# Kernel tuning notes

Hardware: AMD Instinct MI355X
Metric: run time of the kernel (lower is better)

## Reference

```python
import jax, jax.numpy as jnp
import numpy as np

N_NODES = 100000
N_EDGES = 300000
D_IN = 256
HID = 1024
N_CLASSES = 64


def _linear_params(key, d_in, d_out):
    k1, k2 = jax.random.split(key)
    bound = 1.0 / np.sqrt(d_in)
    W = jax.random.uniform(k1, (d_in, d_out), jnp.float32, -bound, bound)
    b = jax.random.uniform(k2, (d_out,), jnp.float32, -bound, bound)
    return W, b


def setup_inputs() -> dict:
    key = jax.random.key(0)
    ks = jax.random.split(key, 8)
    x = jax.random.normal(ks[0], (N_NODES, D_IN), jnp.float32)
    edge_index = jax.random.randint(ks[1], (2, N_EDGES), 0, N_NODES, jnp.int64)
    W1a, b1a = _linear_params(ks[2], D_IN, HID)
    W1b, b1b = _linear_params(ks[3], HID, HID)
    W2a, b2a = _linear_params(ks[4], HID, HID)
    W2b, b2b = _linear_params(ks[5], HID, HID)
    Wfc, bfc = _linear_params(ks[6], HID, N_CLASSES)
    return {"x": x, "edge_index": edge_index,
            "W1a": W1a, "b1a": b1a, "W1b": W1b, "b1b": b1b,
            "W2a": W2a, "b2a": b2a, "W2b": W2b, "b2b": b2b,
            "Wfc": Wfc, "bfc": bfc}


def _gin_conv(x, src, dst, Wa, ba, Wb, bb):
    # GINConv, eps=0: nn(x + sum_{j in N(i)} x_j); messages flow src -> dst.
    agg = jax.ops.segment_sum(x[src], dst, num_segments=N_NODES)
    h = x + agg
    h = jax.nn.relu(h @ Wa + ba)
    return h @ Wb + bb


def reference(x, edge_index, W1a, b1a, W1b, b1b, W2a, b2a, W2b, b2b, Wfc, bfc):
    src, dst = edge_index[0], edge_index[1]
    h = _gin_conv(x, src, dst, W1a, b1a, W1b, b1b)
    h = jax.nn.relu(h)
    h = _gin_conv(h, src, dst, W2a, b2a, W2b, b2b)
    logits = h @ Wfc + bfc
    return jax.nn.log_softmax(logits, axis=1)
```

## Files before the change

kernel.cpp:

```cpp
#include <hip/hip_runtime.h>
#include <stdint.h>

#define N_NODES 100000
#define N_EDGES 300000
#define D_IN 256
#define HID 1024
#define N_CLASSES 64
#define NSCAN ((N_NODES + 1023) / 1024)

typedef __bf16 bf16x8 __attribute__((ext_vector_type(8)));
typedef float f32x4 __attribute__((ext_vector_type(4)));

__device__ __forceinline__ float bf2f(unsigned short u) {
  union { unsigned int i; float f; } v; v.i = ((unsigned int)u) << 16; return v.f;
}
__device__ __forceinline__ unsigned short f2bf(float f) {
  union { float f; unsigned int i; } v; v.f = f;
  unsigned int u = v.i;
  unsigned int r = (u + 0x7FFFu + ((u >> 16) & 1u)) >> 16;
  return (unsigned short)r;
}

__device__ __forceinline__ void async16(const void* g, void* l) {
  __builtin_amdgcn_global_load_lds(
      (const __attribute__((address_space(1))) void*)g,
      (__attribute__((address_space(3))) void*)l, 16, 0, 0);
}

__global__ void probe_flags(const unsigned short* __restrict__ w,
                            const unsigned int* __restrict__ e,
                            int* __restrict__ flags) {
  __shared__ int cnt;
  __shared__ unsigned int orv;
  if (threadIdx.x == 0) { cnt = 0; orv = 0u; }
  __syncthreads();
  int c = 0;
  for (int i = threadIdx.x; i < 4096; i += 256) {
    unsigned int ex = (w[i] >> 7) & 0xFFu;
    if (ex > 123u) ++c;
  }
  atomicAdd(&cnt, c);
  unsigned int o = 0;
  for (int j = threadIdx.x; j < 1000; j += 256) o |= e[2 * j + 1];
  atomicOr(&orv, o);
  __syncthreads();
  if (threadIdx.x == 0) {
    flags[0] = (cnt > 64) ? 1 : 0;
    flags[1] = (orv == 0u) ? 1 : 0;
  }
}

__global__ void cvt_edges(const unsigned int* __restrict__ ei,
                          int* __restrict__ src32, int* __restrict__ dst32,
                          const int* __restrict__ flags) {
  int i = blockIdx.x * 256 + threadIdx.x;
  if (i >= N_EDGES) return;
  if (flags[1]) {
    src32[i] = (int)ei[2 * i];
    dst32[i] = (int)ei[2 * (size_t)N_EDGES + 2 * i];
  } else {
    src32[i] = (int)ei[i];
    dst32[i] = (int)ei[N_EDGES + i];
  }
}

template <int FB16>
__global__ void transpose_tile(const void* __restrict__ W,
                               unsigned short* __restrict__ Wt, int K, int N,
                               const int* __restrict__ flags) {
  __shared__ float t[64][65];
  const int n0 = blockIdx.x * 64, k0 = blockIdx.y * 64;
  const int lane = threadIdx.x & 63, rg = threadIdx.x >> 6;
  const bool isf32 = FB16 ? false : (flags[0] != 0);
#pragma unroll
  for (int i = 0; i < 16; ++i) {
    int r = rg * 16 + i;
    long idx = (long)(k0 + r) * N + n0 + lane;
    t[r][lane] = isf32 ? ((const float*)W)[idx]
                       : bf2f(((const unsigned short*)W)[idx]);
  }
  __syncthreads();
#pragma unroll
  for (int i = 0; i < 16; ++i) {
    int r = rg * 16 + i;
    Wt[(long)(n0 + r) * K + k0 + lane] = f2bf(t[lane][r]);
  }
}

__global__ void cvt_bias_all(const void* __restrict__ b1a, const void* __restrict__ b1b,
                             const void* __restrict__ b2a, const void* __restrict__ b2b,
                             const void* __restrict__ bfc,
                             unsigned short* __restrict__ bb,
                             const int* __restrict__ flags) {
  int i = blockIdx.x * 256 + threadIdx.x;
  if (i >= 4 * HID + N_CLASSES) return;
  const void* src; int off;
  if (i < HID)          { src = b1a; off = i; }
  else if (i < 2 * HID) { src = b1b; off = i - HID; }
  else if (i < 3 * HID) { src = b2a; off = i - 2 * HID; }
  else if (i < 4 * HID) { src = b2b; off = i - 3 * HID; }
  else                  { src = bfc; off = i - 4 * HID; }
  bb[i] = flags[0] ? f2bf(((const float*)src)[off])
                   : ((const unsigned short*)src)[off];
}

__global__ void bcomb_kernel(const unsigned short* __restrict__ bb2b,
                             const unsigned short* __restrict__ WfcT,
                             const unsigned short* __restrict__ bbfc,
                             unsigned short* __restrict__ bcomb) {
  int c = threadIdx.x;
  if (c >= N_CLASSES) return;
  float s = bf2f(bbfc[c]);
  for (int j = 0; j < HID; ++j)
    s += bf2f(bb2b[j]) * bf2f(WfcT[(long)c * HID + j]);
  bcomb[c] = f2bf(s);
}

__global__ void hist_deg(const int* __restrict__ dst, int* __restrict__ deg) {
  int e = blockIdx.x * 256 + threadIdx.x;
  if (e < N_EDGES) atomicAdd(&deg[dst[e]], 1);
}

__global__ void scan_part(const int* __restrict__ deg, int* __restrict__ rowptr,
                          int* __restrict__ bsum) {
  __shared__ int lds[1024];
  int i = blockIdx.x * 1024 + threadIdx.x;
  int v = (i < N_NODES) ? deg[i] : 0;
  lds[threadIdx.x] = v;
  __syncthreads();
  for (int off = 1; off < 1024; off <<= 1) {
    int t = (threadIdx.x >= off) ? lds[threadIdx.x - off] : 0;
    __syncthreads();
    lds[threadIdx.x] += t;
    __syncthreads();
  }
  if (i < N_NODES) rowptr[i + 1] = lds[threadIdx.x];
  if (threadIdx.x == 1023) bsum[blockIdx.x] = lds[1023];
}

__global__ void scan_top(int* __restrict__ bsum) {
  __shared__ int lds[128];
  int v = (threadIdx.x < NSCAN) ? bsum[threadIdx.x] : 0;
  lds[threadIdx.x] = v;
  __syncthreads();
  for (int off = 1; off < 128; off <<= 1) {
    int t = (threadIdx.x >= off) ? lds[threadIdx.x - off] : 0;
    __syncthreads();
    lds[threadIdx.x] += t;
    __syncthreads();
  }
  if (threadIdx.x < NSCAN) bsum[threadIdx.x] = lds[threadIdx.x] - v;
}

__global__ void scan_fix(const int* __restrict__ deg, int* __restrict__ rowptr,
                         int* __restrict__ cursor, const int* __restrict__ bsum) {
  int i = blockIdx.x * 1024 + threadIdx.x;
  if (i < N_NODES) {
    int incl = rowptr[i + 1] + bsum[blockIdx.x];
    rowptr[i + 1] = incl;
    cursor[i] = incl - deg[i];
  }
  if (i == 0) rowptr[0] = 0;
}

__global__ void fill_csr(const int* __restrict__ src, const int* __restrict__ dst,
                         int* __restrict__ cursor, int* __restrict__ csr) {
  int e = blockIdx.x * 256 + threadIdx.x;
  if (e < N_EDGES) {
    int pos = atomicAdd(&cursor[dst[e]], 1);
    csr[pos] = src[e];
  }
}

__global__ void agg1_full(const void* __restrict__ X,
                          const int* __restrict__ rowptr,
                          const int* __restrict__ csr,
                          unsigned short* __restrict__ h,
                          const int* __restrict__ flags) {
  int node = blockIdx.x * 4 + (threadIdx.x >> 6);
  int lane = threadIdx.x & 63;
  if (node >= N_NODES) return;
  bool isf32 = flags[0] != 0;
  float acc[4];
  int e0 = rowptr[node], e1 = rowptr[node + 1];
  if (isf32) {
    const float* Xf = (const float*)X;
    float4 v = ((const float4*)(Xf + (long)node * D_IN))[lane];
    acc[0] = v.x; acc[1] = v.y; acc[2] = v.z; acc[3] = v.w;
    int j = e0;
    for (; j + 3 < e1; j += 4) {
      int s0 = csr[j], s1 = csr[j + 1], s2 = csr[j + 2], s3 = csr[j + 3];
      float4 v0 = ((const float4*)(Xf + (long)s0 * D_IN))[lane];
      float4 v1 = ((const float4*)(Xf + (long)s1 * D_IN))[lane];
      float4 v2 = ((const float4*)(Xf + (long)s2 * D_IN))[lane];
      float4 v3 = ((const float4*)(Xf + (long)s3 * D_IN))[lane];
      acc[0] += v0.x; acc[1] += v0.y; acc[2] += v0.z; acc[3] += v0.w;
      acc[0] += v1.x; acc[1] += v1.y; acc[2] += v1.z; acc[3] += v1.w;
      acc[0] += v2.x; acc[1] += v2.y; acc[2] += v2.z; acc[3] += v2.w;
      acc[0] += v3.x; acc[1] += v3.y; acc[2] += v3.z; acc[3] += v3.w;
    }
    for (; j < e1; ++j) {
      int s = csr[j];
      float4 v0 = ((const float4*)(Xf + (long)s * D_IN))[lane];
      acc[0] += v0.x; acc[1] += v0.y; acc[2] += v0.z; acc[3] += v0.w;
    }
  } else {
    const unsigned short* Xb = (const unsigned short*)X;
    ushort4 v = ((const ushort4*)(Xb + (long)node * D_IN))[lane];
    acc[0] = bf2f(v.x); acc[1] = bf2f(v.y); acc[2] = bf2f(v.z); acc[3] = bf2f(v.w);
    int j = e0;
    for (; j + 3 < e1; j += 4) {
      int s0 = csr[j], s1 = csr[j + 1], s2 = csr[j + 2], s3 = csr[j + 3];
      ushort4 v0 = ((const ushort4*)(Xb + (long)s0 * D_IN))[lane];
      ushort4 v1 = ((const ushort4*)(Xb + (long)s1 * D_IN))[lane];
      ushort4 v2 = ((const ushort4*)(Xb + (long)s2 * D_IN))[lane];
      ushort4 v3 = ((const ushort4*)(Xb + (long)s3 * D_IN))[lane];
      acc[0] += bf2f(v0.x); acc[1] += bf2f(v0.y); acc[2] += bf2f(v0.z); acc[3] += bf2f(v0.w);
      acc[0] += bf2f(v1.x); acc[1] += bf2f(v1.y); acc[2] += bf2f(v1.z); acc[3] += bf2f(v1.w);
      acc[0] += bf2f(v2.x); acc[1] += bf2f(v2.y); acc[2] += bf2f(v2.z); acc[3] += bf2f(v2.w);
      acc[0] += bf2f(v3.x); acc[1] += bf2f(v3.y); acc[2] += bf2f(v3.z); acc[3] += bf2f(v3.w);
    }
    for (; j < e1; ++j) {
      int s = csr[j];
      ushort4 v0 = ((const ushort4*)(Xb + (long)s * D_IN))[lane];
      acc[0] += bf2f(v0.x); acc[1] += bf2f(v0.y); acc[2] += bf2f(v0.z); acc[3] += bf2f(v0.w);
    }
  }
  ushort4 o;
  o.x = f2bf(acc[0]); o.y = f2bf(acc[1]); o.z = f2bf(acc[2]); o.w = f2bf(acc[3]);
  ((ushort4*)(h + (long)node * D_IN))[lane] = o;
}

__global__ void agg2_rot(const unsigned short* __restrict__ Q,
                         const int* __restrict__ rowptr,
                         const int* __restrict__ csr,
                         unsigned short* __restrict__ out, long ostride, int cb) {
  int node = blockIdx.x * 4 + (threadIdx.x >> 6);
  int lane = threadIdx.x & 63;
  if (node >= N_NODES) return;
  unsigned int p = ((const unsigned int*)(Q + (long)node * HID + cb * 128))[lane];
  float a0 = bf2f((unsigned short)(p & 0xFFFFu));
  float a1 = bf2f((unsigned short)(p >> 16));
  int e0 = rowptr[node], e1 = rowptr[node + 1];
  int j = e0;
  for (; j + 1 < e1; j += 2) {
    int s0 = csr[j], s1 = csr[j + 1];
    unsigned int q0 = ((const unsigned int*)(Q + (long)s0 * HID + cb * 128))[lane];
    unsigned int q1 = ((const unsigned int*)(Q + (long)s1 * HID + cb * 128))[lane];
    a0 += bf2f((unsigned short)(q0 & 0xFFFFu));
    a1 += bf2f((unsigned short)(q0 >> 16));
    a0 += bf2f((unsigned short)(q1 & 0xFFFFu));
    a1 += bf2f((unsigned short)(q1 >> 16));
  }
  if (j < e1) {
    int s = csr[j];
    unsigned int q = ((const unsigned int*)(Q + (long)s * HID + cb * 128))[lane];
    a0 += bf2f((unsigned short)(q & 0xFFFFu));
    a1 += bf2f((unsigned short)(q >> 16));
  }
  unsigned int o = (unsigned int)f2bf(a0) | ((unsigned int)f2bf(a1) << 16);
  ((unsigned int*)(out + (long)node * ostride))[lane] = o;
}

__global__ void copyback_cols(unsigned short* __restrict__ Q,
                              const unsigned short* __restrict__ T, int cb) {
  long i = (long)blockIdx.x * 256 + threadIdx.x;
  if (i < (long)N_NODES * 16) {
    long node = i >> 4;
    int c = (int)(i & 15);
    ((uint4*)(Q + node * HID + cb * 128))[c] = ((const uint4*)T)[i];
  }
}

template <int WGM, int WGN, int EPI>
__global__ __launch_bounds__(256, 2) void gemm_bt(
    const unsigned short* __restrict__ A, const unsigned short* __restrict__ Bt,
    const unsigned short* __restrict__ bias, void* __restrict__ Cout,
    int M, int N, int K, int akoff) {
  constexpr int BM = WGM * 64;
  constexpr int BN = WGN * 64;
  __shared__ alignas(16) unsigned short ldsA[BM * 64];
  __shared__ alignas(16) unsigned short ldsB[BN * 64];
  const int tid = threadIdx.x;
  const int lane = tid & 63;
  const int w = tid >> 6;
  const int wm = w % WGM;
  const int wn = w / WGM;
  const long row0 = (long)blockIdx.x * BM;
  const long col0 = (long)blockIdx.y * BN;
  const int l15 = lane & 15, lq = lane >> 4;

  f32x4 acc[4][4];
#pragma unroll
  for (int i = 0; i < 4; ++i)
#pragma unroll
    for (int j = 0; j < 4; ++j) acc[i][j] = f32x4{0.f, 0.f, 0.f, 0.f};

  for (int k0 = 0; k0 < K; k0 += 64) {
    const int ka = (k0 + akoff) & (K - 1);
#pragma unroll
    for (int i = 0; i < BM * 8 / 256; ++i) {
      int t = i * 256 + tid;
      int r = t >> 3, c = t & 7;
      long gr = row0 + r;
      if (gr >= M) gr = M - 1;
      const unsigned short* g = A + gr * (long)K + ka + ((c ^ (r & 7)) << 3);
      void* l = (char*)ldsA + (size_t)(i * 256 + (tid & ~63)) * 16;
      async16(g, l);
    }
#pragma unroll
    for (int i = 0; i < BN * 8 / 256; ++i) {
      int t = i * 256 + tid;
      int r = t >> 3, c = t & 7;
      long gr = col0 + r;
      const unsigned short* g = Bt + gr * (long)K + k0 + ((c ^ (r & 7)) << 3);
      void* l = (char*)ldsB + (size_t)(i * 256 + (tid & ~63)) * 16;
      async16(g, l);
    }
    __syncthreads();
#pragma unroll
    for (int kk = 0; kk < 64; kk += 32) {
      bf16x8 av[4], bv[4];
#pragma unroll
      for (int mt = 0; mt < 4; ++mt) {
        int m = wm * 64 + mt * 16 + l15;
        int jj = ((kk >> 3) + lq) ^ (m & 7);
        av[mt] = *(const bf16x8*)(ldsA + m * 64 + jj * 8);
      }
#pragma unroll
      for (int nt = 0; nt < 4; ++nt) {
        int n = wn * 64 + nt * 16 + l15;
        int jj = ((kk >> 3) + lq) ^ (n & 7);
        bv[nt] = *(const bf16x8*)(ldsB + n * 64 + jj * 8);
      }
#pragma unroll
      for (int mt = 0; mt < 4; ++mt)
#pragma unroll
        for (int nt = 0; nt < 4; ++nt)
          acc[mt][nt] = __builtin_amdgcn_mfma_f32_16x16x32_bf16(
              av[mt], bv[nt], acc[mt][nt], 0, 0, 0);
    }
    __syncthreads();
  }

  if (EPI == 3) {
    float bvx[4];
#pragma unroll
    for (int nt = 0; nt < 4; ++nt) bvx[nt] = bf2f(bias[wn * 64 + nt * 16 + l15]);
#pragma unroll
    for (int mt = 0; mt < 4; ++mt) {
#pragma unroll
      for (int r = 0; r < 4; ++r) {
        long gm = row0 + wm * 64 + mt * 16 + lq * 4 + r;
        float v[4];
#pragma unroll
        for (int nt = 0; nt < 4; ++nt) v[nt] = acc[mt][nt][r] + bvx[nt];
        float mx = fmaxf(fmaxf(v[0], v[1]), fmaxf(v[2], v[3]));
#pragma unroll
        for (int o = 1; o < 16; o <<= 1) mx = fmaxf(mx, __shfl_xor(mx, o, 16));
        float s = expf(v[0] - mx) + expf(v[1] - mx) + expf(v[2] - mx) + expf(v[3] - mx);
#pragma unroll
        for (int o = 1; o < 16; o <<= 1) s += __shfl_xor(s, o, 16);
        float ls = logf(s);
        if (gm < M) {
#pragma unroll
          for (int nt = 0; nt < 4; ++nt)
            ((float*)Cout)[gm * N + nt * 16 + l15] = v[nt] - mx - ls;
        }
      }
    }
    return;
  }

#pragma unroll
  for (int nt = 0; nt < 4; ++nt) {
    long gn = col0 + wn * 64 + nt * 16 + l15;
    float bvl = bf2f(bias[gn]);
#pragma unroll
    for (int mt = 0; mt < 4; ++mt) {
      long gm0 = row0 + wm * 64 + mt * 16 + lq * 4;
#pragma unroll
      for (int r = 0; r < 4; ++r) {
        long gm = gm0 + r;
        if (gm < M) {
          float v = acc[mt][nt][r] + bvl;
          if (EPI == 1) v = v > 0.f ? v : 0.f;
          if (EPI == 2)
            ((float*)Cout)[gm * N + gn] = v;
          else
            ((unsigned short*)Cout)[gm * N + gn] = f2bf(v);
        }
      }
    }
  }
}

extern "C" void kernel_launch(void* const* d_in, const int* in_sizes, int n_in,
                              void* d_out, int out_size, void* d_ws,
                              size_t ws_size, hipStream_t stream) {
  const void* x = d_in[0];
  const unsigned int* ei = (const unsigned int*)d_in[1];
  const void* W1a = d_in[2];
  const void* b1a = d_in[3];
  const void* W1b = d_in[4];
  const void* b1b = d_in[5];
  const void* W2a = d_in[6];
  const void* b2a = d_in[7];
  const void* W2b = d_in[8];
  const void* b2b = d_in[9];
  const void* Wfc = d_in[10];
  const void* bfc = d_in[11];
  (void)n_in; (void)in_sizes; (void)out_size;

  const size_t BIG_NEED = 246909600;
  const bool big = (ws_size >= BIG_NEED);
  const int CMr = big ? 16384 : 8192;
  const int NFULLr = big ? 6 : 12;
  const int TAILR = N_NODES - NFULLr * CMr;

  char* wsb = (char*)d_ws;
  const size_t HOFF = (size_t)N_NODES * (HID - D_IN);
  const size_t AGG_OFF = 204800000;
  const size_t W_OFFv = big ? 238354432 : 233600000;
  const size_t WBYTES = 6946816;
  const size_t B_OFFv = W_OFFv + WBYTES;
  const size_t RP_OFFv = B_OFFv + 8320;
  const size_t CSR_OFFv = RP_OFFv + 400016;
  const size_t F_OFFv = CSR_OFFv + 1200000;
  unsigned short* Q = (unsigned short*)(wsb + 0);
  unsigned short* hQ = Q + HOFF;
  unsigned short* T1 = (unsigned short*)(wsb + AGG_OFF);
  int* src32 = (int*)(wsb + AGG_OFF);
  int* dst32 = src32 + N_EDGES;
  int* deg = dst32 + N_EDGES;
  int* cursor = deg + N_NODES;
  int* bsum = (int*)(wsb + AGG_OFF + 4 * 1024 * 1024);
  unsigned short* W2bN = (unsigned short*)(wsb + AGG_OFF + 25600000);
  unsigned short* WcombT = (unsigned short*)(wsb + AGG_OFF + 25600000 + 2097152);
  unsigned short* bcomb = WcombT + (size_t)N_CLASSES * HID;
  unsigned short* zbias = bcomb + 64;
  unsigned short* W1aT = (unsigned short*)(wsb + W_OFFv);
  unsigned short* W1bT = W1aT + (size_t)D_IN * HID;
  unsigned short* W2aT = W1bT + (size_t)HID * HID;
  unsigned short* W2bT = W2aT + (size_t)HID * HID;
  unsigned short* WfcT = W2bT + (size_t)HID * HID;
  unsigned short* bb1a = (unsigned short*)(wsb + B_OFFv);
  unsigned short* bb1b = bb1a + HID;
  unsigned short* bb2a = bb1b + HID;
  unsigned short* bb2b = bb2a + HID;
  unsigned short* bbfc = bb2b + HID;
  int* rowptr = (int*)(wsb + RP_OFFv);
  int* csr = (int*)(wsb + CSR_OFFv);
  int* flags = (int*)(wsb + F_OFFv);

  probe_flags<<<1, 256, 0, stream>>>((const unsigned short*)W1a, ei, flags);
  cvt_edges<<<(N_EDGES + 255) / 256, 256, 0, stream>>>(ei, src32, dst32, flags);
  hipMemsetAsync(deg, 0, (size_t)N_NODES * 4, stream);
  hist_deg<<<(N_EDGES + 255) / 256, 256, 0, stream>>>(dst32, deg);
  scan_part<<<NSCAN, 1024, 0, stream>>>(deg, rowptr, bsum);
  scan_top<<<1, 128, 0, stream>>>(bsum);
  scan_fix<<<NSCAN, 1024, 0, stream>>>(deg, rowptr, cursor, bsum);
  fill_csr<<<(N_EDGES + 255) / 256, 256, 0, stream>>>(src32, dst32, cursor, csr);
  cvt_bias_all<<<(4 * HID + N_CLASSES + 255) / 256, 256, 0, stream>>>(
      b1a, b1b, b2a, b2b, bfc, bb1a, flags);
  transpose_tile<0><<<dim3(HID / 64, D_IN / 64), 256, 0, stream>>>(W1a, W1aT, D_IN, HID, flags);
  transpose_tile<0><<<dim3(HID / 64, HID / 64), 256, 0, stream>>>(W1b, W1bT, HID, HID, flags);
  transpose_tile<0><<<dim3(HID / 64, HID / 64), 256, 0, stream>>>(W2a, W2aT, HID, HID, flags);
  transpose_tile<0><<<dim3(HID / 64, HID / 64), 256, 0, stream>>>(W2b, W2bT, HID, HID, flags);
  transpose_tile<0><<<dim3(N_CLASSES / 64, HID / 64), 256, 0, stream>>>(Wfc, WfcT, HID, N_CLASSES, flags);

  const int ngrid = (N_NODES + 3) / 4;

  agg1_full<<<ngrid, 256, 0, stream>>>(x, rowptr, csr, hQ, flags);

  for (int c = 0; c <= NFULLr; ++c) {
    int rows = (c < NFULLr) ? CMr : TAILR;
    if (rows <= 0) break;
    const unsigned short* Ac = hQ + (size_t)c * CMr * D_IN;
    unsigned short* Qc = Q + (size_t)c * CMr * HID;
    dim3 g((rows + 127) / 128, HID / 128);
    gemm_bt<2, 2, 1><<<g, 256, 0, stream>>>(Ac, W1aT, bb1a, T1, rows, HID, D_IN, 0);
    gemm_bt<2, 2, 1><<<g, 256, 0, stream>>>(T1, W1bT, bb1b, Qc, rows, HID, HID, 0);
  }

  hipMemsetAsync(zbias, 0, 2048, stream);
  transpose_tile<1><<<dim3(HID / 64, HID / 64), 256, 0, stream>>>(W2bT, W2bN, HID, HID, flags);
  gemm_bt<1, 4, 0><<<dim3(1, 4), 256, 0, stream>>>(WfcT, W2bN, zbias, WcombT, 64, HID, HID, 0);
  bcomb_kernel<<<1, 64, 0, stream>>>(bb2b, WfcT, bbfc, bcomb);

  for (int cb = 0; cb < HID / 128; ++cb) {
    if (cb == 0)
      agg2_rot<<<ngrid, 256, 0, stream>>>(Q, rowptr, csr, T1, 128, 0);
    else
      agg2_rot<<<ngrid, 256, 0, stream>>>(Q, rowptr, csr,
                                          Q + (size_t)(cb - 1) * 128, HID, cb);
  }
  const int cgrid = (int)(((long)N_NODES * 16 + 255) / 256);
  copyback_cols<<<cgrid, 256, 0, stream>>>(Q, T1, 7);

  const int CH2 = 12288, NF2 = 8;
  for (int c = 0; c <= NF2; ++c) {
    int rows = (c < NF2) ? CH2 : (N_NODES - NF2 * CH2);
    if (rows <= 0) break;
    unsigned short* Qc = Q + (size_t)c * CH2 * HID;
    dim3 g((rows + 127) / 128, HID / 128);
    gemm_bt<2, 2, 1><<<g, 256, 0, stream>>>(Qc, W2aT, bb2a, T1, rows, HID, HID, 896);
    dim3 gh((rows + 255) / 256, 1);
    gemm_bt<4, 1, 3><<<gh, 256, 0, stream>>>(
        T1, WcombT, bcomb, (float*)d_out + (size_t)c * CH2 * N_CLASSES,
        rows, N_CLASSES, HID, 0);
  }
}
```

Before: 1.574 ms.

## Add unchunked full-workspace path and batch head GEMM over whole output

Result: faster. 1.372 ms (-12.9%).

```diff
diff --git a/kernel.cpp b/kernel.cpp
--- a/kernel.cpp
+++ b/kernel.cpp
@@ -231,6 +231,65 @@
   ((ushort4*)(h + (long)node * D_IN))[lane] = o;
 }
 
+__device__ __forceinline__ void add8(float* a, unsigned int x, unsigned int y,
+                                     unsigned int z, unsigned int w) {
+  a[0] += bf2f((unsigned short)(x & 0xFFFFu)); a[1] += bf2f((unsigned short)(x >> 16));
+  a[2] += bf2f((unsigned short)(y & 0xFFFFu)); a[3] += bf2f((unsigned short)(y >> 16));
+  a[4] += bf2f((unsigned short)(z & 0xFFFFu)); a[5] += bf2f((unsigned short)(z >> 16));
+  a[6] += bf2f((unsigned short)(w & 0xFFFFu)); a[7] += bf2f((unsigned short)(w >> 16));
+}
+
+__global__ void agg2_full(const unsigned short* __restrict__ Qin,
+                          const int* __restrict__ rowptr,
+                          const int* __restrict__ csr,
+                          unsigned short* __restrict__ Uout) {
+  int node = blockIdx.x * 4 + (threadIdx.x >> 6);
+  int lane = threadIdx.x & 63;
+  if (node >= N_NODES) return;
+  float acc[16];
+  {
+    const uint4* row = (const uint4*)(Qin + (long)node * HID);
+    uint4 a = row[lane], b = row[64 + lane];
+    acc[0] = bf2f((unsigned short)(a.x & 0xFFFFu)); acc[1] = bf2f((unsigned short)(a.x >> 16));
+    acc[2] = bf2f((unsigned short)(a.y & 0xFFFFu)); acc[3] = bf2f((unsigned short)(a.y >> 16));
+    acc[4] = bf2f((unsigned short)(a.z & 0xFFFFu)); acc[5] = bf2f((unsigned short)(a.z >> 16));
+    acc[6] = bf2f((unsigned short)(a.w & 0xFFFFu)); acc[7] = bf2f((unsigned short)(a.w >> 16));
+    acc[8] = bf2f((unsigned short)(b.x & 0xFFFFu)); acc[9] = bf2f((unsigned short)(b.x >> 16));
+    acc[10] = bf2f((unsigned short)(b.y & 0xFFFFu)); acc[11] = bf2f((unsigned short)(b.y >> 16));
+    acc[12] = bf2f((unsigned short)(b.z & 0xFFFFu)); acc[13] = bf2f((unsigned short)(b.z >> 16));
+    acc[14] = bf2f((unsigned short)(b.w & 0xFFFFu)); acc[15] = bf2f((unsigned short)(b.w >> 16));
+  }
+  int e0 = rowptr[node], e1 = rowptr[node + 1];
+  int j = e0;
+  for (; j + 1 < e1; j += 2) {
+    const uint4* r0 = (const uint4*)(Qin + (long)csr[j] * HID);
+    const uint4* r1 = (const uint4*)(Qin + (long)csr[j + 1] * HID);
+    uint4 a0 = r0[lane], b0 = r0[64 + lane];
+    uint4 a1 = r1[lane], b1 = r1[64 + lane];
+    add8(acc, a0.x, a0.y, a0.z, a0.w);
+    add8(acc + 8, b0.x, b0.y, b0.z, b0.w);
+    add8(acc, a1.x, a1.y, a1.z, a1.w);
+    add8(acc + 8, b1.x, b1.y, b1.z, b1.w);
+  }
+  if (j < e1) {
+    const uint4* r0 = (const uint4*)(Qin + (long)csr[j] * HID);
+    uint4 a0 = r0[lane], b0 = r0[64 + lane];
+    add8(acc, a0.x, a0.y, a0.z, a0.w);
+    add8(acc + 8, b0.x, b0.y, b0.z, b0.w);
+  }
+  uint4 oa, ob;
+  oa.x = (unsigned)f2bf(acc[0]) | ((unsigned)f2bf(acc[1]) << 16);
+  oa.y = (unsigned)f2bf(acc[2]) | ((unsigned)f2bf(acc[3]) << 16);
+  oa.z = (unsigned)f2bf(acc[4]) | ((unsigned)f2bf(acc[5]) << 16);
+  oa.w = (unsigned)f2bf(acc[6]) | ((unsigned)f2bf(acc[7]) << 16);
+  ob.x = (unsigned)f2bf(acc[8]) | ((unsigned)f2bf(acc[9]) << 16);
+  ob.y = (unsigned)f2bf(acc[10]) | ((unsigned)f2bf(acc[11]) << 16);
+  ob.z = (unsigned)f2bf(acc[12]) | ((unsigned)f2bf(acc[13]) << 16);
+  ob.w = (unsigned)f2bf(acc[14]) | ((unsigned)f2bf(acc[15]) << 16);
+  uint4* orow = (uint4*)(Uout + (long)node * HID);
+  orow[lane] = oa; orow[64 + lane] = ob;
+}
+
 __global__ void agg2_rot(const unsigned short* __restrict__ Q,
                          const int* __restrict__ rowptr,
                          const int* __restrict__ csr,
@@ -243,20 +302,21 @@
   float a1 = bf2f((unsigned short)(p >> 16));
   int e0 = rowptr[node], e1 = rowptr[node + 1];
   int j = e0;
-  for (; j + 1 < e1; j += 2) {
-    int s0 = csr[j], s1 = csr[j + 1];
+  for (; j + 3 < e1; j += 4) {
+    int s0 = csr[j], s1 = csr[j + 1], s2 = csr[j + 2], s3 = csr[j + 3];
     unsigned int q0 = ((const unsigned int*)(Q + (long)s0 * HID + cb * 128))[lane];
     unsigned int q1 = ((const unsigned int*)(Q + (long)s1 * HID + cb * 128))[lane];
-    a0 += bf2f((unsigned short)(q0 & 0xFFFFu));
-    a1 += bf2f((unsigned short)(q0 >> 16));
-    a0 += bf2f((unsigned short)(q1 & 0xFFFFu));
-    a1 += bf2f((unsigned short)(q1 >> 16));
-  }
-  if (j < e1) {
+    unsigned int q2 = ((const unsigned int*)(Q + (long)s2 * HID + cb * 128))[lane];
+    unsigned int q3 = ((const unsigned int*)(Q + (long)s3 * HID + cb * 128))[lane];
+    a0 += bf2f((unsigned short)(q0 & 0xFFFFu)); a1 += bf2f((unsigned short)(q0 >> 16));
+    a0 += bf2f((unsigned short)(q1 & 0xFFFFu)); a1 += bf2f((unsigned short)(q1 >> 16));
+    a0 += bf2f((unsigned short)(q2 & 0xFFFFu)); a1 += bf2f((unsigned short)(q2 >> 16));
+    a0 += bf2f((unsigned short)(q3 & 0xFFFFu)); a1 += bf2f((unsigned short)(q3 >> 16));
+  }
+  for (; j < e1; ++j) {
     int s = csr[j];
     unsigned int q = ((const unsigned int*)(Q + (long)s * HID + cb * 128))[lane];
-    a0 += bf2f((unsigned short)(q & 0xFFFFu));
-    a1 += bf2f((unsigned short)(q >> 16));
+    a0 += bf2f((unsigned short)(q & 0xFFFFu)); a1 += bf2f((unsigned short)(q >> 16));
   }
   unsigned int o = (unsigned int)f2bf(a0) | ((unsigned int)f2bf(a1) << 16);
   ((unsigned int*)(out + (long)node * ostride))[lane] = o;
@@ -412,14 +472,78 @@
   const void* bfc = d_in[11];
   (void)n_in; (void)in_sizes; (void)out_size;
 
+  char* wsb = (char*)d_ws;
+  const size_t HOFF = (size_t)N_NODES * (HID - D_IN);
+  const size_t HUGE_NEED = 420385568;
   const size_t BIG_NEED = 246909600;
+
+  if (ws_size >= HUGE_NEED) {
+    const size_t U_OFF = 204800000;
+    const size_t W_OFF3 = 409600000;
+    unsigned short* Q = (unsigned short*)(wsb + 0);
+    unsigned short* hQ = Q + HOFF;
+    unsigned short* U = (unsigned short*)(wsb + U_OFF);
+    int* src32 = (int*)(wsb + U_OFF);
+    int* dst32 = src32 + N_EDGES;
+    int* deg = dst32 + N_EDGES;
+    int* cursor = deg + N_NODES;
+    int* bsum = (int*)(wsb + U_OFF + 4 * 1024 * 1024);
+    unsigned short* W1aT = (unsigned short*)(wsb + W_OFF3);
+    unsigned short* W1bT = W1aT + (size_t)D_IN * HID;
+    unsigned short* W2aT = W1bT + (size_t)HID * HID;
+    unsigned short* W2bT = W2aT + (size_t)HID * HID;
+    unsigned short* WfcT = W2bT + (size_t)HID * HID;
+    unsigned short* bb1a = WfcT + (size_t)HID * N_CLASSES;
+    unsigned short* bb1b = bb1a + HID;
+    unsigned short* bb2a = bb1b + HID;
+    unsigned short* bb2b = bb2a + HID;
+    unsigned short* bbfc = bb2b + HID;
+    unsigned short* W2bN = bbfc + N_CLASSES;
+    unsigned short* WcombT = W2bN + (size_t)HID * HID;
+    unsigned short* bcomb = WcombT + (size_t)N_CLASSES * HID;
+    unsigned short* zbias = bcomb + 64;
+    int* rowptr = (int*)(zbias + 1024);
+    int* csr = rowptr + N_NODES + 4;
+    int* flags = csr + N_EDGES;
+
+    probe_flags<<<1, 256, 0, stream>>>((const unsigned short*)W1a, ei, flags);
+    cvt_edges<<<(N_EDGES + 255) / 256, 256, 0, stream>>>(ei, src32, dst32, flags);
+    hipMemsetAsync(deg, 0, (size_t)N_NODES * 4, stream);
+    hist_deg<<<(N_EDGES + 255) / 256, 256, 0, stream>>>(dst32, deg);
+    scan_part<<<NSCAN, 1024, 0, stream>>>(deg, rowptr, bsum);
+    scan_top<<<1, 128, 0, stream>>>(bsum);
+    scan_fix<<<NSCAN, 1024, 0, stream>>>(deg, rowptr, cursor, bsum);
+    fill_csr<<<(N_EDGES + 255) / 256, 256, 0, stream>>>(src32, dst32, cursor, csr);
+    cvt_bias_all<<<(4 * HID + N_CLASSES + 255) / 256, 256, 0, stream>>>(
+        b1a, b1b, b2a, b2b, bfc, bb1a, flags);
+    transpose_tile<0><<<dim3(HID / 64, D_IN / 64), 256, 0, stream>>>(W1a, W1aT, D_IN, HID, flags);
+    transpose_tile<0><<<dim3(HID / 64, HID / 64), 256, 0, stream>>>(W1b, W1bT, HID, HID, flags);
+    transpose_tile<0><<<dim3(HID / 64, HID / 64), 256, 0, stream>>>(W2a, W2aT, HID, HID, flags);
+    transpose_tile<0><<<dim3(HID / 64, HID / 64), 256, 0, stream>>>(W2b, W2bT, HID, HID, flags);
+    transpose_tile<0><<<dim3(N_CLASSES / 64, HID / 64), 256, 0, stream>>>(Wfc, WfcT, HID, N_CLASSES, flags);
+    hipMemsetAsync(zbias, 0, 2048, stream);
+    transpose_tile<1><<<dim3(HID / 64, HID / 64), 256, 0, stream>>>(W2bT, W2bN, HID, HID, flags);
+    gemm_bt<1, 4, 0><<<dim3(1, 4), 256, 0, stream>>>(WfcT, W2bN, zbias, WcombT, 64, HID, HID, 0);
+    bcomb_kernel<<<1, 64, 0, stream>>>(bb2b, WfcT, bbfc, bcomb);
+
+    const int ngrid = (N_NODES + 3) / 4;
+    agg1_full<<<ngrid, 256, 0, stream>>>(x, rowptr, csr, hQ, flags);
+    dim3 gfull((N_NODES + 127) / 128, HID / 128);
+    gemm_bt<2, 2, 1><<<gfull, 256, 0, stream>>>(hQ, W1aT, bb1a, U, N_NODES, HID, D_IN, 0);
+    gemm_bt<2, 2, 1><<<gfull, 256, 0, stream>>>(U, W1bT, bb1b, Q, N_NODES, HID, HID, 0);
+    agg2_full<<<ngrid, 256, 0, stream>>>(Q, rowptr, csr, U);
+    gemm_bt<2, 2, 1><<<gfull, 256, 0, stream>>>(U, W2aT, bb2a, Q, N_NODES, HID, HID, 0);
+    dim3 ghead((N_NODES + 255) / 256, 1);
+    gemm_bt<4, 1, 3><<<ghead, 256, 0, stream>>>(
+        Q, WcombT, bcomb, (float*)d_out, N_NODES, N_CLASSES, HID, 0);
+    return;
+  }
+
   const bool big = (ws_size >= BIG_NEED);
   const int CMr = big ? 16384 : 8192;
   const int NFULLr = big ? 6 : 12;
   const int TAILR = N_NODES - NFULLr * CMr;
 
-  char* wsb = (char*)d_ws;
-  const size_t HOFF = (size_t)N_NODES * (HID - D_IN);
   const size_t AGG_OFF = 204800000;
   const size_t W_OFFv = big ? 238354432 : 233600000;
   const size_t WBYTES = 6946816;
@@ -470,7 +594,6 @@
   transpose_tile<0><<<dim3(N_CLASSES / 64, HID / 64), 256, 0, stream>>>(Wfc, WfcT, HID, N_CLASSES, flags);
 
   const int ngrid = (N_NODES + 3) / 4;
-
   agg1_full<<<ngrid, 256, 0, stream>>>(x, rowptr, csr, hQ, flags);
 
   for (int c = 0; c <= NFULLr; ++c) {
@@ -503,11 +626,16 @@
     int rows = (c < NF2) ? CH2 : (N_NODES - NF2 * CH2);
     if (rows <= 0) break;
     unsigned short* Qc = Q + (size_t)c * CH2 * HID;
+    unsigned short* out = (c == 0) ? T1 : Q + (size_t)(c - 1) * CH2 * HID;
     dim3 g((rows + 127) / 128, HID / 128);
-    gemm_bt<2, 2, 1><<<g, 256, 0, stream>>>(Qc, W2aT, bb2a, T1, rows, HID, HID, 896);
-    dim3 gh((rows + 255) / 256, 1);
-    gemm_bt<4, 1, 3><<<gh, 256, 0, stream>>>(
-        T1, WcombT, bcomb, (float*)d_out + (size_t)c * CH2 * N_CLASSES,
-        rows, N_CLASSES, HID, 0);
-  }
-}
+    gemm_bt<2, 2, 1><<<g, 256, 0, stream>>>(Qc, W2aT, bb2a, out, rows, HID, HID, 896);
+  }
+  dim3 gh1((CH2 + 255) / 256, 1);
+  gemm_bt<4, 1, 3><<<gh1, 256, 0, stream>>>(
+      T1, WcombT, bcomb, (float*)d_out, CH2, N_CLASSES, HID, 0);
+  const int rem = N_NODES - CH2;
+  dim3 gh2((rem + 255) / 256, 1);
+  gemm_bt<4, 1, 3><<<gh2, 256, 0, stream>>>(
+      Q, WcombT, bcomb, (float*)d_out + (size_t)CH2 * N_CLASSES,
+      rem, N_CLASSES, HID, 0);
+}
```
